# Kernel tuning notes

Measured on AMD Instinct MI355X. Metric: run time of the kernel, lower is better.

## Reference

```python
import jax, jax.numpy as jnp
from jax import lax
import numpy as np

EPS_LN = 1e-5
EPS_BN = 1e-5


def _forward(x, prior, alpha, in_proj_w, conv_w, conv_b, x_proj_weight,
             dt_projs_weight, dt_projs_bias, A_logs, Ds, out_norm_w, out_norm_b,
             out_proj_w, p2w_w1, p2w_b1, p2w_bn_w, p2w_bn_b, p2w_bn_mean,
             p2w_bn_var, p2w_w2, p2w_b2):
    Din = conv_w.shape[0]
    # in_proj (Linear2d == 1x1 conv), split into ssm branch and gate z
    xz = jnp.einsum('bchw,dc->bdhw', x, in_proj_w)          # [B, 2*Din, H, W]
    x_ssm, z = jnp.split(xz, 2, axis=1)
    # depthwise 3x3 conv + SiLU
    x_ssm = lax.conv_general_dilated(
        x_ssm, conv_w, (1, 1), 'SAME',
        dimension_numbers=('NCHW', 'OIHW', 'NCHW'),
        feature_group_count=Din) + conv_b[None, :, None, None]
    x_ssm = jax.nn.silu(x_ssm)

    B, D, H, W = x_ssm.shape
    L = H * W
    K = 4
    R = dt_projs_weight.shape[2]
    N = A_logs.shape[1]

    # cross_scan: 4 directions = row-major, col-major, and their reverses
    row = x_ssm.reshape(B, D, L)
    col = x_ssm.transpose(0, 1, 3, 2).reshape(B, D, L)
    xs = jnp.stack([row, col, row[..., ::-1], col[..., ::-1]], axis=1)  # [B,K,D,L]

    x_dbl = jnp.einsum('bkdl,kcd->bkcl', xs, x_proj_weight)  # [B,K,R+2N,L]
    dts, Bs, Cs = jnp.split(x_dbl, [R, R + N], axis=2)       # [B,K,R,L],[B,K,N,L],[B,K,N,L]
    dts = jnp.einsum('bkrl,kdr->bkdl', dts, dt_projs_weight)  # [B,K,D,L]

    A = -jnp.exp(A_logs.astype(jnp.float32)).reshape(K, D, N)
    dt = jax.nn.softplus(dts + dt_projs_bias[None, :, :, None])  # [B,K,D,L]

    dA = jnp.exp(dt[..., None] * A[None, :, :, None, :])          # [B,K,D,L,N]
    dBx = dt[..., None] * Bs.transpose(0, 1, 3, 2)[:, :, None, :, :] * xs[..., None]
    Cseq = Cs.transpose(0, 1, 3, 2)                               # [B,K,L,N]

    dA_t = jnp.moveaxis(dA, 3, 0)    # [L,B,K,D,N]
    dBx_t = jnp.moveaxis(dBx, 3, 0)  # [L,B,K,D,N]
    C_t = jnp.moveaxis(Cseq, 2, 0)   # [L,B,K,N]

    def step(h, inp):
        a, bx, c = inp
        h = h * a + bx                              # [B,K,D,N]
        y = jnp.einsum('bkdn,bkn->bkd', h, c)
        return h, y

    h0 = jnp.zeros((B, K, D, N), dtype=jnp.float32)
    _, ys = lax.scan(step, h0, (dA_t, dBx_t, C_t))  # [L,B,K,D]
    ys = jnp.moveaxis(ys, 0, 3)                     # [B,K,D,L]
    ys = ys + Ds.reshape(K, D)[None, :, :, None] * xs
    ys = ys.reshape(B, K, D, H, W)

    # prior -> per-direction guidance weights (PriorToWeights, BN in eval mode)
    g = jnp.einsum('bchw,oc->bohw', prior, p2w_w1) + p2w_b1[None, :, None, None]
    g = (g - p2w_bn_mean[None, :, None, None]) * jax.lax.rsqrt(
        p2w_bn_var[None, :, None, None] + EPS_BN)
    g = g * p2w_bn_w[None, :, None, None] + p2w_bn_b[None, :, None, None]
    g = jax.nn.relu(g)
    g = jnp.einsum('bchw,oc->bohw', g, p2w_w2) + p2w_b2[None, :, None, None]
    gw = jax.nn.sigmoid(g)                          # [B,4,H,W]
    s = jax.nn.sigmoid(alpha)                       # [1]
    Wdir = 1.0 + s * (gw - 1.0)                     # torch.lerp(ones, gw, s)
    ys = ys * Wdir[:, :, None, :, :]

    # cross_merge: inverse of cross_scan, sum of 4 directions
    ysl = ys.reshape(B, K, D, L)
    y = ysl[:, 0] + ysl[:, 2, :, ::-1]
    yt = ysl[:, 1] + ysl[:, 3, :, ::-1]
    y = y + yt.reshape(B, D, W, H).transpose(0, 1, 3, 2).reshape(B, D, L)
    y = y.reshape(B, D, H, W)

    # LayerNorm2d: normalize over channel dim
    mu = y.mean(axis=1, keepdims=True)
    var = y.var(axis=1, keepdims=True)
    y = (y - mu) * jax.lax.rsqrt(var + EPS_LN)
    y = y * out_norm_w[None, :, None, None] + out_norm_b[None, :, None, None]

    y = y * jax.nn.silu(z)
    out = jnp.einsum('bdhw,md->bmhw', y, out_proj_w)  # out_proj 1x1, no bias
    return out


def setup_inputs() -> dict:
    key = jax.random.key(0)
    ks = jax.random.split(key, 16)
    B, Dm, H, W = 8, 96, 64, 64
    Din, N, K, R, hid = 192, 1, 4, 6, 32

    def rn(k, shape, scale):
        return jax.random.normal(k, shape, jnp.float32) * scale

    return {
        'x': rn(ks[0], (B, Dm, H, W), 1.0),
        'prior': jax.random.uniform(ks[1], (B, 4, H, W), jnp.float32),
        'alpha': rn(ks[2], (1,), 1.0),
        'in_proj_w': rn(ks[3], (2 * Din, Dm), Dm ** -0.5),
        'conv_w': rn(ks[4], (Din, 1, 3, 3), 1.0 / 3.0),
        'conv_b': rn(ks[5], (Din,), 0.1),
        'x_proj_weight': rn(ks[6], (K, R + 2 * N, Din), Din ** -0.5),
        'dt_projs_weight': rn(ks[7], (K, Din, R), R ** -0.5),
        'dt_projs_bias': rn(ks[8], (K, Din), 0.5) - 4.0,
        'A_logs': jnp.tile(jnp.log(jnp.arange(1, N + 1, dtype=jnp.float32)), (K * Din, 1)),
        'Ds': jnp.ones((K * Din,), jnp.float32),
        'out_norm_w': jnp.ones((Din,), jnp.float32),
        'out_norm_b': jnp.zeros((Din,), jnp.float32),
        'out_proj_w': rn(ks[9], (Dm, Din), Din ** -0.5),
        'p2w_w1': rn(ks[10], (hid, 4), 0.5),
        'p2w_b1': jnp.zeros((hid,), jnp.float32),
        'p2w_bn_w': jnp.ones((hid,), jnp.float32),
        'p2w_bn_b': jnp.zeros((hid,), jnp.float32),
        'p2w_bn_mean': jnp.zeros((hid,), jnp.float32),
        'p2w_bn_var': jnp.ones((hid,), jnp.float32),
        'p2w_w2': rn(ks[11], (4, hid), hid ** -0.5),
        'p2w_b2': jnp.zeros((4,), jnp.float32),
    }


def reference(x, prior, alpha, in_proj_w, conv_w, conv_b, x_proj_weight,
              dt_projs_weight, dt_projs_bias, A_logs, Ds, out_norm_w, out_norm_b,
              out_proj_w, p2w_w1, p2w_b1, p2w_bn_w, p2w_bn_b, p2w_bn_mean,
              p2w_bn_var, p2w_w2, p2w_b2):
    return _forward(x, prior, alpha, in_proj_w, conv_w, conv_b, x_proj_weight,
                    dt_projs_weight, dt_projs_bias, A_logs, Ds, out_norm_w,
                    out_norm_b, out_proj_w, p2w_w1, p2w_b1, p2w_bn_w, p2w_bn_b,
                    p2w_bn_mean, p2w_bn_var, p2w_w2, p2w_b2)
```

## Files before the change

kernel.cpp:

```cpp
#include <hip/hip_runtime.h>

#define BB   8
#define CIN  96
#define DIN  192
#define HH   64
#define WW   64
#define LL   4096
#define KK   4
#define COUT 96
#define SS   128
#define LC   32

#define LOG2E 1.4426950408889634f
#define LN2   0.6931471805599453f

typedef unsigned short bf16t;
typedef float f32x2 __attribute__((ext_vector_type(2)));
typedef float f32x4 __attribute__((ext_vector_type(4)));
typedef short bf16x8s __attribute__((ext_vector_type(8)));

__device__ __forceinline__ f32x2 pkfma(f32x2 a, f32x2 b, f32x2 c) {
#if __has_builtin(__builtin_elementwise_fma)
  return __builtin_elementwise_fma(a, b, c);
#else
  f32x2 r;
  r[0] = fmaf(a[0], b[0], c[0]);
  r[1] = fmaf(a[1], b[1], c[1]);
  return r;
#endif
}

__device__ __forceinline__ float exp2fast(float x) { return __builtin_amdgcn_exp2f(x); }
__device__ __forceinline__ float log2fast(float x) { return __builtin_amdgcn_logf(x); }
__device__ __forceinline__ float sigf(float x) { return 1.0f / (1.0f + __expf(-x)); }
__device__ __forceinline__ int trp(int p) { return ((p & 63) << 6) | (p >> 6); }
__device__ __forceinline__ int pix_of(int k, int l) {
  if (k == 0) return l;
  if (k == 1) return trp(l);
  if (k == 2) return LL - 1 - l;
  return trp(LL - 1 - l);
}
__device__ __forceinline__ float b2f(bf16t v) {
  return __uint_as_float((unsigned)v << 16);
}
__device__ __forceinline__ bf16t f2b(float f) {
  unsigned u = __float_as_uint(f);
  return (bf16t)((u + 0x7FFFu + ((u >> 16) & 1u)) >> 16);
}

__global__ __launch_bounds__(256) void gemm_in_mfma_k(const float* __restrict__ x,
                                                      const bf16t* __restrict__ Wb,
                                                      bf16t* __restrict__ out) {
  __shared__ bf16t ldsB[32 * 104];
  const int tid = threadIdx.x;
  const int b = blockIdx.z;
  const int p0 = blockIdx.x * 32;
  for (int idx = tid; idx < CIN * 32; idx += 256) {
    int c = idx >> 5, px = idx & 31;
    ldsB[px * 104 + c] = f2b(x[((size_t)b * CIN + c) * LL + p0 + px]);
  }
  __syncthreads();
  const int wave = tid >> 6, lane = tid & 63;
  const int lm = lane & 15, kc = lane >> 4;
  bf16x8s bfrag[2][3];
#pragma unroll
  for (int nf = 0; nf < 2; ++nf)
#pragma unroll
    for (int ks = 0; ks < 3; ++ks)
      bfrag[nf][ks] = *(const bf16x8s*)&ldsB[(nf * 16 + lm) * 104 + ks * 32 + kc * 8];
  bf16t* ob = out + (size_t)b * 384 * LL + p0;
#pragma unroll
  for (int mti = 0; mti < 6; ++mti) {
    const int o0 = (wave * 6 + mti) * 16;
    bf16x8s afrag[3];
#pragma unroll
    for (int ks = 0; ks < 3; ++ks)
      afrag[ks] = *(const bf16x8s*)&Wb[(size_t)(o0 + lm) * CIN + ks * 32 + kc * 8];
    f32x4 acc0 = {0.f, 0.f, 0.f, 0.f};
    f32x4 acc1 = {0.f, 0.f, 0.f, 0.f};
#pragma unroll
    for (int ks = 0; ks < 3; ++ks) {
      acc0 = __builtin_amdgcn_mfma_f32_16x16x32_bf16(afrag[ks], bfrag[0][ks], acc0, 0, 0, 0);
      acc1 = __builtin_amdgcn_mfma_f32_16x16x32_bf16(afrag[ks], bfrag[1][ks], acc1, 0, 0, 0);
    }
#pragma unroll
    for (int r = 0; r < 4; ++r) {
      ob[(size_t)(o0 + kc * 4 + r) * LL + lm]      = f2b(acc0[r]);
      ob[(size_t)(o0 + kc * 4 + r) * LL + 16 + lm] = f2b(acc1[r]);
    }
  }
}

__global__ __launch_bounds__(384) void ln_gemm_out_k(const bf16t* __restrict__ ymT,
                                                     const bf16t* __restrict__ ymT2,
                                                     const bf16t* __restrict__ xz,
                                                     const float* __restrict__ gamma,
                                                     const float* __restrict__ beta,
                                                     const bf16t* __restrict__ Wh,
                                                     const bf16t* __restrict__ Wl,
                                                     float* __restrict__ out) {
  __shared__ bf16t ldsB[64 * 200];
  __shared__ float sS[6][64], sQ[6][64];
  const int tid = threadIdx.x;
  const int b = blockIdx.z;
  const int h = blockIdx.x;
  const int p0 = h * 64;
  const bf16t* ymb = ymT + (size_t)b * (384 * (size_t)LL);
  for (int idx = tid; idx < 64 * DIN; idx += 384) {
    int pp = idx / DIN, dd = idx % DIN;
    float v = b2f(ymb[(size_t)(p0 + pp) * DIN + dd]) +
              b2f(ymT2[((size_t)b * LL + pp * 64 + h) * DIN + dd]);
    ldsB[pp * 200 + dd] = f2b(v);
  }
  __syncthreads();
  const int px = tid & 63, g = tid >> 6;
  float sum = 0.0f, ss = 0.0f;
  for (int dd = g * 32; dd < g * 32 + 32; ++dd) {
    float v = b2f(ldsB[px * 200 + dd]);
    sum += v;
    ss = fmaf(v, v, ss);
  }
  sS[g][px] = sum;
  sQ[g][px] = ss;
  __syncthreads();
  sum = 0.0f; ss = 0.0f;
#pragma unroll
  for (int gg = 0; gg < 6; ++gg) { sum += sS[gg][px]; ss += sQ[gg][px]; }
  const float mu = sum * (1.0f / DIN);
  float var = ss * (1.0f / DIN) - mu * mu;
  const float rstd = rsqrtf(fmaxf(var, 0.0f) + 1e-5f);
  const bf16t* zb = xz + ((size_t)b * 384 + DIN) * LL + p0 + px;
  for (int dd = g * 32; dd < g * 32 + 32; ++dd) {
    float v = b2f(ldsB[px * 200 + dd]);
    float z = b2f(zb[(size_t)dd * LL]);
    float tn = fmaf((v - mu) * rstd, gamma[dd], beta[dd]);
    ldsB[px * 200 + dd] = f2b(tn * (z * sigf(z)));
  }
  __syncthreads();
  const int wave = tid / 64, lane = tid & 63;
  const int lm = lane & 15, kc = lane >> 4;
  const int o0 = wave * 16;
  bf16x8s ah[6], al[6];
#pragma unroll
  for (int ks = 0; ks < 6; ++ks) {
    ah[ks] = *(const bf16x8s*)&Wh[(size_t)(o0 + lm) * DIN + ks * 32 + kc * 8];
    al[ks] = *(const bf16x8s*)&Wl[(size_t)(o0 + lm) * DIN + ks * 32 + kc * 8];
  }
  float* ob = out + (size_t)b * COUT * LL + p0;
#pragma unroll
  for (int nf = 0; nf < 4; ++nf) {
    f32x4 acc = {0.f, 0.f, 0.f, 0.f};
#pragma unroll
    for (int ks = 0; ks < 6; ++ks) {
      bf16x8s bfr = *(const bf16x8s*)&ldsB[(nf * 16 + lm) * 200 + ks * 32 + kc * 8];
      acc = __builtin_amdgcn_mfma_f32_16x16x32_bf16(ah[ks], bfr, acc, 0, 0, 0);
      acc = __builtin_amdgcn_mfma_f32_16x16x32_bf16(al[ks], bfr, acc, 0, 0, 0);
    }
#pragma unroll
    for (int r = 0; r < 4; ++r)
      ob[(size_t)(o0 + kc * 4 + r) * LL + nf * 16 + lm] = acc[r];
  }
}

__global__ __launch_bounds__(256) void p2w_k(const float* __restrict__ prior,
                                             const float* __restrict__ alpha,
                                             const float* __restrict__ w1,
                                             const float* __restrict__ b1,
                                             const float* __restrict__ bnw,
                                             const float* __restrict__ bnb,
                                             const float* __restrict__ bnm,
                                             const float* __restrict__ bnv,
                                             const float* __restrict__ w2,
                                             const float* __restrict__ b2,
                                             const float* __restrict__ xpw,
                                             const float* __restrict__ ipw,
                                             const float* __restrict__ opw,
                                             float* __restrict__ xpwT,
                                             bf16t* __restrict__ ipwb,
                                             bf16t* __restrict__ opwbh,
                                             bf16t* __restrict__ opwbl,
                                             float* __restrict__ Wg) {
  if (blockIdx.x == 0) {
    for (int idx = threadIdx.x; idx < KK * DIN * 8; idx += 256) {
      int kk = idx / (DIN * 8);
      int rem = idx % (DIN * 8);
      int dd = rem >> 3, c = rem & 7;
      xpwT[idx] = xpw[(kk * 8 + c) * DIN + dd];
    }
  }
  if (blockIdx.x == 1) {
    for (int idx = threadIdx.x; idx < 384 * CIN; idx += 256)
      ipwb[idx] = f2b(ipw[idx]);
  }
  if (blockIdx.x == 2) {
    for (int idx = threadIdx.x; idx < COUT * DIN; idx += 256) {
      float w = opw[idx];
      bf16t hi = f2b(w);
      opwbh[idx] = hi;
      opwbl[idx] = f2b(w - b2f(hi));
    }
  }
  int idx = blockIdx.x * 256 + threadIdx.x;
  int p = idx & (LL - 1);
  int b = idx >> 12;
  float pr[4];
#pragma unroll
  for (int c = 0; c < 4; ++c) pr[c] = prior[((size_t)b * 4 + c) * LL + p];
  float s = sigf(alpha[0]);
  float g2[4];
#pragma unroll
  for (int j = 0; j < 4; ++j) g2[j] = b2[j];
  for (int o = 0; o < 32; ++o) {
    float g = b1[o];
#pragma unroll
    for (int c = 0; c < 4; ++c) g = fmaf(pr[c], w1[o * 4 + c], g);
    g = (g - bnm[o]) * rsqrtf(bnv[o] + 1e-5f) * bnw[o] + bnb[o];
    g = fmaxf(g, 0.0f);
#pragma unroll
    for (int j = 0; j < 4; ++j) g2[j] = fmaf(g, w2[j * 32 + o], g2[j]);
  }
#pragma unroll
  for (int j = 0; j < 4; ++j)
    Wg[((size_t)b * 4 + j) * LL + p] = 1.0f + s * (sigf(g2[j]) - 1.0f);
}

__global__ __launch_bounds__(1024) void convproj_k(const bf16t* __restrict__ xz,
                                                   const float* __restrict__ cw,
                                                   const float* __restrict__ cb,
                                                   const float* __restrict__ xpwT,
                                                   bf16t* __restrict__ xcT,
                                                   float* __restrict__ projS) {
  __shared__ float sX[96 * 65];
  __shared__ float4 sP[512];
  const int tid = threadIdx.x;
  const int b = blockIdx.y;
  const int h = blockIdx.x;
  const int px = tid & 63;
  const int ku = __builtin_amdgcn_readfirstlane((tid >> 6) & 3);
  const int hf = __builtin_amdgcn_readfirstlane((tid >> 8) & 1);
  const int q  = __builtin_amdgcn_readfirstlane(tid >> 9);
  f32x2 a01 = {0.f, 0.f}, a23 = {0.f, 0.f};

#pragma unroll
  for (int half = 0; half < 2; ++half) {
    for (int idx = tid; idx < 96 * 16; idx += 1024) {
      int ddl = idx >> 4, pq = idx & 15;
      int w0 = pq * 4;
      int dd = half * 96 + ddl;
      const bf16t* base = xz + ((size_t)b * 384 + dd) * LL + h * 64 + w0;
      const float* wp = cw + dd * 9;
      float bv = cb[dd];
      f32x2 s01 = {bv, bv}, s23 = {bv, bv};
#pragma unroll
      for (int dh = -1; dh <= 1; ++dh) {
        int hh = h + dh;
        if (hh < 0 || hh >= HH) continue;
        const bf16t* row = base + dh * 64;
        ushort4 cmu = *(const ushort4*)row;
        float cmx = b2f(cmu.x), cmy = b2f(cmu.y), cmz = b2f(cmu.z), cmw = b2f(cmu.w);
        float lf = (w0 > 0)  ? b2f(row[-1]) : 0.0f;
        float rt = (w0 < 60) ? b2f(row[4])  : 0.0f;
        float c0 = wp[(dh + 1) * 3], c1 = wp[(dh + 1) * 3 + 1], c2 = wp[(dh + 1) * 3 + 2];
        s01 = pkfma((f32x2){lf,  cmx}, (f32x2){c0, c0}, s01);
        s01 = pkfma((f32x2){cmx, cmy}, (f32x2){c1, c1}, s01);
        s01 = pkfma((f32x2){cmy, cmz}, (f32x2){c2, c2}, s01);
        s23 = pkfma((f32x2){cmy, cmz}, (f32x2){c0, c0}, s23);
        s23 = pkfma((f32x2){cmz, cmw}, (f32x2){c1, c1}, s23);
        s23 = pkfma((f32x2){cmw, rt},  (f32x2){c2, c2}, s23);
      }
      float* so = &sX[ddl * 65 + w0];
      float v0 = s01[0], v1 = s01[1], v2 = s23[0], v3 = s23[1];
      so[0] = v0 * sigf(v0);
      so[1] = v1 * sigf(v1);
      so[2] = v2 * sigf(v2);
      so[3] = v3 * sigf(v3);
    }
    __syncthreads();
    for (int idx = tid; idx < 64 * 96; idx += 1024) {
      int pp = idx / 96, ddl = idx % 96;
      xcT[((size_t)b * LL + h * 64 + pp) * DIN + half * 96 + ddl] =
          f2b(sX[ddl * 65 + pp]);
    }
    {
      const int ddl0 = q * 48;
      const float* wp = xpwT + (size_t)ku * (DIN * 8) + (half * 96 + ddl0) * 8 + hf * 4;
#pragma unroll 8
      for (int d48 = 0; d48 < 48; ++d48) {
        float xv = sX[(ddl0 + d48) * 65 + px];
        const float4 w4 = *(const float4*)(wp + d48 * 8);
        const f32x2 xv2 = {xv, xv};
        a01 = pkfma(xv2, (f32x2){w4.x, w4.y}, a01);
        a23 = pkfma(xv2, (f32x2){w4.z, w4.w}, a23);
      }
    }
    __syncthreads();
  }
  const int slot = tid & 511;
  if (q == 1) sP[slot] = make_float4(a01[0], a01[1], a23[0], a23[1]);
  __syncthreads();
  if (q == 0) {
    float4 o = sP[slot];
    float r0 = a01[0] + o.x, r1 = a01[1] + o.y, r2 = a23[0] + o.z, r3 = a23[1] + o.w;
    const int p = h * 64 + px;
    int l;
    if (ku == 0) l = p;
    else if (ku == 1) l = trp(p);
    else if (ku == 2) l = LL - 1 - p;
    else l = LL - 1 - trp(p);
    float* pb = projS + (((size_t)b * KK + ku) * LL + l) * 8 + hf * 4;
    *(float4*)pb = make_float4(r0, r1, r2, r3);
  }
}

__global__ __launch_bounds__(192) void scan_part_k(const bf16t* __restrict__ xcT,
                                                   const float* __restrict__ projS,
                                                   const float* __restrict__ dtw,
                                                   const float* __restrict__ dtb,
                                                   const float* __restrict__ A_logs,
                                                   float* __restrict__ carrP,
                                                   float* __restrict__ carrH) {
  const int s = blockIdx.x, kp = blockIdx.y, b = blockIdx.z;
  const int d = threadIdx.x;
  const int kA = kp, kB = kp + 2;
  const int s2 = SS - 1 - s;
  const int kdA = kA * DIN + d, kdB = kB * DIN + d;
  float wrA[6], wrB[6];
#pragma unroll
  for (int r = 0; r < 6; ++r) { wrA[r] = dtw[kdA * 6 + r]; wrB[r] = dtw[kdB * 6 + r]; }
  const float biasA = dtb[kdA], biasB = dtb[kdB];
  const float AaA = -__expf(A_logs[kdA]), AaB = -__expf(A_logs[kdB]);
  const int l0 = s * LC;
  const int p0 = pix_of(kA, l0);
  const int dp = pix_of(kA, l0 + 1) - p0;
  const bf16t* xp = xcT + ((size_t)b * LL + p0) * DIN + d;
  const long xstep = (long)dp * DIN;
  const float* prA = projS + (((size_t)b * KK + kA) * LL + l0) * 8;
  const float* prB = projS + (((size_t)b * KK + kB) * LL + s2 * LC + (LC - 1)) * 8;
  float PA = 1.0f, HA = 0.0f, PB = 1.0f, HB = 0.0f;
#pragma unroll 2
  for (int j = 0; j < LC; ++j) {
    float4 a0 = *(const float4*)prA;
    float4 a1 = *(const float4*)(prA + 4);
    prA += 8;
    float4 b0 = *(const float4*)prB;
    float4 b1 = *(const float4*)(prB + 4);
    prB -= 8;
    float xv = b2f(*xp);
    xp += xstep;
    {
      float dtr = biasA;
      dtr = fmaf(a0.x, wrA[0], dtr);
      dtr = fmaf(a0.y, wrA[1], dtr);
      dtr = fmaf(a0.z, wrA[2], dtr);
      dtr = fmaf(a0.w, wrA[3], dtr);
      dtr = fmaf(a1.x, wrA[4], dtr);
      dtr = fmaf(a1.y, wrA[5], dtr);
      float e = exp2fast(fminf(dtr, 80.0f) * LOG2E);
      float u = log2fast(1.0f + e);
      float a = exp2fast(u * AaA);
      float dt = u * LN2;
      HA = fmaf(a, HA, dt * a1.z * xv);
      PA *= a;
    }
    {
      float dtr = biasB;
      dtr = fmaf(b0.x, wrB[0], dtr);
      dtr = fmaf(b0.y, wrB[1], dtr);
      dtr = fmaf(b0.z, wrB[2], dtr);
      dtr = fmaf(b0.w, wrB[3], dtr);
      dtr = fmaf(b1.x, wrB[4], dtr);
      dtr = fmaf(b1.y, wrB[5], dtr);
      float e = exp2fast(fminf(dtr, 80.0f) * LOG2E);
      float u = log2fast(1.0f + e);
      float a = exp2fast(u * AaB);
      float dt = u * LN2;
      HB = fmaf(PB, dt * b1.z * xv, HB);
      PB *= a;
    }
  }
  size_t oA = ((size_t)((b * KK + kA) * SS + s)) * DIN + d;
  size_t oB = ((size_t)((b * KK + kB) * SS + s2)) * DIN + d;
  carrP[oA] = PA;
  carrH[oA] = HA;
  carrP[oB] = PB;
  carrH[oB] = HB;
}

__global__ __launch_bounds__(192) void scan_fix_k(const float* __restrict__ carrP,
                                                  const float* __restrict__ carrH,
                                                  float* __restrict__ h0) {
  const int k = blockIdx.x, b = blockIdx.y, d = threadIdx.x;
  size_t base = ((size_t)(b * KK + k)) * SS * DIN + d;
  float h = 0.0f;
#pragma unroll 4
  for (int s = 0; s < SS; ++s) {
    h0[base + (size_t)s * DIN] = h;
    h = fmaf(carrP[base + (size_t)s * DIN], h, carrH[base + (size_t)s * DIN]);
  }
}

__global__ __launch_bounds__(192) void scan_apply_k(const bf16t* __restrict__ xcT,
                                                    const float* __restrict__ projS,
                                                    const float* __restrict__ Wg,
                                                    const float* __restrict__ h0,
                                                    const float* __restrict__ dtw,
                                                    const float* __restrict__ dtb,
                                                    const float* __restrict__ A_logs,
                                                    const float* __restrict__ Ds,
                                                    bf16t* __restrict__ ymT,
                                                    bf16t* __restrict__ ymT2) {
  const int s = blockIdx.x, kp = blockIdx.y, b = blockIdx.z;
  const int d = threadIdx.x;
  __shared__ float sAcc[LC * DIN];
  float xr[LC];
  {
    const int k = kp, kd = k * DIN + d;
    float wr[6];
#pragma unroll
    for (int r = 0; r < 6; ++r) wr[r] = dtw[kd * 6 + r];
    const float bias = dtb[kd];
    const float Aa = -__expf(A_logs[kd]);
    const float Dv = Ds[kd];
    const int l0 = s * LC;
    const int p0 = pix_of(k, l0);
    const int dp = pix_of(k, l0 + 1) - p0;
    const bf16t* xp = xcT + ((size_t)b * LL + p0) * DIN + d;
    const long xstep = (long)dp * DIN;
    const float* pr = projS + (((size_t)b * KK + k) * LL + l0) * 8;
    const float* wg = Wg + ((size_t)b * KK + k) * LL + l0;
    float h = h0[((size_t)((b * KK + k) * SS + s)) * DIN + d];
#pragma unroll
    for (int j = 0; j < LC; ++j) {
      float4 q0 = *(const float4*)pr;
      float4 q1 = *(const float4*)(pr + 4);
      pr += 8;
      float xv = b2f(*xp);
      xp += xstep;
      xr[j] = xv;
      float dtr = bias;
      dtr = fmaf(q0.x, wr[0], dtr);
      dtr = fmaf(q0.y, wr[1], dtr);
      dtr = fmaf(q0.z, wr[2], dtr);
      dtr = fmaf(q0.w, wr[3], dtr);
      dtr = fmaf(q1.x, wr[4], dtr);
      dtr = fmaf(q1.y, wr[5], dtr);
      float e = exp2fast(fminf(dtr, 80.0f) * LOG2E);
      float u = log2fast(1.0f + e);
      float a = exp2fast(u * Aa);
      float dt = u * LN2;
      h = fmaf(a, h, dt * q1.z * xv);
      sAcc[j * DIN + d] = fmaf(h, q1.w, Dv * xv) * wg[j];
    }
  }
  {
    const int k = kp + 2, kd = k * DIN + d;
    const int s2 = SS - 1 - s;
    float wr[6];
#pragma unroll
    for (int r = 0; r < 6; ++r) wr[r] = dtw[kd * 6 + r];
    const float bias = dtb[kd];
    const float Aa = -__expf(A_logs[kd]);
    const float Dv = Ds[kd];
    const int l0 = s2 * LC;
    const float* pr = projS + (((size_t)b * KK + k) * LL + l0) * 8;
    const float* wg = Wg + ((size_t)b * KK + k) * LL + l0;
    float h = h0[((size_t)((b * KK + k) * SS + s2)) * DIN + d];
#pragma unroll
    for (int j = 0; j < LC; ++j) {
      float4 q0 = *(const float4*)pr;
      float4 q1 = *(const float4*)(pr + 4);
      pr += 8;
      float xv = xr[LC - 1 - j];
      float dtr = bias;
      dtr = fmaf(q0.x, wr[0], dtr);
      dtr = fmaf(q0.y, wr[1], dtr);
      dtr = fmaf(q0.z, wr[2], dtr);
      dtr = fmaf(q0.w, wr[3], dtr);
      dtr = fmaf(q1.x, wr[4], dtr);
      dtr = fmaf(q1.y, wr[5], dtr);
      float e = exp2fast(fminf(dtr, 80.0f) * LOG2E);
      float u = log2fast(1.0f + e);
      float a = exp2fast(u * Aa);
      float dt = u * LN2;
      h = fmaf(a, h, dt * q1.z * xv);
      float y = fmaf(h, q1.w, Dv * xv) * wg[j];
      sAcc[(LC - 1 - j) * DIN + d] += y;
    }
  }
  bf16t* dst;
  if (kp == 0)
    dst = ymT + (size_t)b * (384 * (size_t)LL) + (size_t)(s * LC) * DIN + d;
  else
    dst = ymT2 + ((size_t)b * LL + s * LC) * DIN + d;
#pragma unroll 4
  for (int j = 0; j < LC; ++j) dst[(size_t)j * DIN] = f2b(sAcc[j * DIN + d]);
}

extern "C" void kernel_launch(void* const* d_in, const int* in_sizes, int n_in,
                              void* d_out, int out_size, void* d_ws, size_t ws_size,
                              hipStream_t stream) {
  const float* x      = (const float*)d_in[0];
  const float* prior  = (const float*)d_in[1];
  const float* alpha  = (const float*)d_in[2];
  const float* ipw    = (const float*)d_in[3];
  const float* cw     = (const float*)d_in[4];
  const float* cb     = (const float*)d_in[5];
  const float* xpw    = (const float*)d_in[6];
  const float* dtw    = (const float*)d_in[7];
  const float* dtb    = (const float*)d_in[8];
  const float* A_logs = (const float*)d_in[9];
  const float* Ds     = (const float*)d_in[10];
  const float* onw    = (const float*)d_in[11];
  const float* onb    = (const float*)d_in[12];
  const float* opw    = (const float*)d_in[13];
  const float* w1     = (const float*)d_in[14];
  const float* b1     = (const float*)d_in[15];
  const float* bnw    = (const float*)d_in[16];
  const float* bnb    = (const float*)d_in[17];
  const float* bnm    = (const float*)d_in[18];
  const float* bnv    = (const float*)d_in[19];
  const float* w2     = (const float*)d_in[20];
  const float* b2     = (const float*)d_in[21];
  float* out = (float*)d_out;

  char* ws = (char*)d_ws;
  bf16t* xz    = (bf16t*)(ws);
  bf16t* xcT   = (bf16t*)(ws + 25165824);
  bf16t* ymT2  = (bf16t*)(ws + 37748736);
  float* projS = (float*)(ws + 50331648);
  float* Wgb   = (float*)(ws + 54525952);
  float* carrP = (float*)(ws + 55050240);
  float* carrH = (float*)(ws + 58195968);
  float* h0b   = (float*)(ws + 61341696);
  float* xpwT  = (float*)(ws + 64487424);
  bf16t* ipwb  = (bf16t*)(ws + 64512000);
  bf16t* opwbh = (bf16t*)(ws + 64585728);
  bf16t* opwbl = (bf16t*)(ws + 64622592);
  bf16t* ymT   = xz;

  p2w_k<<<(BB * LL) / 256, 256, 0, stream>>>(prior, alpha, w1, b1, bnw, bnb, bnm,
                                             bnv, w2, b2, xpw, ipw, opw, xpwT,
                                             ipwb, opwbh, opwbl, Wgb);
  gemm_in_mfma_k<<<dim3(LL / 32, 1, BB), 256, 0, stream>>>(x, ipwb, xz);
  convproj_k<<<dim3(HH, BB), 1024, 0, stream>>>(xz, cw, cb, xpwT, xcT, projS);
  scan_part_k<<<dim3(SS, 2, BB), 192, 0, stream>>>(xcT, projS, dtw, dtb, A_logs,
                                                   carrP, carrH);
  scan_fix_k<<<dim3(KK, BB), 192, 0, stream>>>(carrP, carrH, h0b);
  scan_apply_k<<<dim3(SS, 2, BB), 192, 0, stream>>>(xcT, projS, Wgb, h0b, dtw, dtb,
                                                    A_logs, Ds, ymT, ymT2);
  ln_gemm_out_k<<<dim3(LL / 64, 1, BB), 384, 0, stream>>>(ymT, ymT2, xz, onw, onb,
                                                          opwbh, opwbl, out);
}
```

Baseline: 154.3 us.

## Compute x_proj with bf16 MFMA using hi/lo weight split in convproj

Replaces the scalar packed-FMA x_proj projection in convproj_k with bf16 MFMA 16x16x32 instructions. The x_proj weights are split into bf16 high and low parts to keep accuracy close to fp32 on the weight side. The activations are staged once as bf16 in shared memory, laid out pixel-major, and that tile feeds both the vectorised xcT store and the MFMA B operand. The block shrinks from 1024 to 512 threads and the two-half loop plus cross-half reduction go away. In exchange the activations are rounded to bf16 before the projection, and projS is now written with scalar stores.

```diff
diff --git a/kernel.cpp b/kernel.cpp
--- a/kernel.cpp
+++ b/kernel.cpp
@@ -175,17 +175,18 @@
                                              const float* __restrict__ xpw,
                                              const float* __restrict__ ipw,
                                              const float* __restrict__ opw,
-                                             float* __restrict__ xpwT,
+                                             bf16t* __restrict__ xpwbh,
+                                             bf16t* __restrict__ xpwbl,
                                              bf16t* __restrict__ ipwb,
                                              bf16t* __restrict__ opwbh,
                                              bf16t* __restrict__ opwbl,
                                              float* __restrict__ Wg) {
   if (blockIdx.x == 0) {
-    for (int idx = threadIdx.x; idx < KK * DIN * 8; idx += 256) {
-      int kk = idx / (DIN * 8);
-      int rem = idx % (DIN * 8);
-      int dd = rem >> 3, c = rem & 7;
-      xpwT[idx] = xpw[(kk * 8 + c) * DIN + dd];
+    for (int idx = threadIdx.x; idx < 32 * DIN; idx += 256) {
+      float w = xpw[idx];
+      bf16t hi = f2b(w);
+      xpwbh[idx] = hi;
+      xpwbl[idx] = f2b(w - b2f(hi));
     }
   }
   if (blockIdx.x == 1) {
@@ -224,91 +225,81 @@
     Wg[((size_t)b * 4 + j) * LL + p] = 1.0f + s * (sigf(g2[j]) - 1.0f);
 }
 
-__global__ __launch_bounds__(1024) void convproj_k(const bf16t* __restrict__ xz,
-                                                   const float* __restrict__ cw,
-                                                   const float* __restrict__ cb,
-                                                   const float* __restrict__ xpwT,
-                                                   bf16t* __restrict__ xcT,
-                                                   float* __restrict__ projS) {
-  __shared__ float sX[96 * 65];
-  __shared__ float4 sP[512];
+__global__ __launch_bounds__(512) void convproj_k(const bf16t* __restrict__ xz,
+                                                  const float* __restrict__ cw,
+                                                  const float* __restrict__ cb,
+                                                  const bf16t* __restrict__ Wh,
+                                                  const bf16t* __restrict__ Wl,
+                                                  bf16t* __restrict__ xcT,
+                                                  float* __restrict__ projS) {
+  __shared__ bf16t sXb[64 * 200];
   const int tid = threadIdx.x;
   const int b = blockIdx.y;
   const int h = blockIdx.x;
-  const int px = tid & 63;
-  const int ku = __builtin_amdgcn_readfirstlane((tid >> 6) & 3);
-  const int hf = __builtin_amdgcn_readfirstlane((tid >> 8) & 1);
-  const int q  = __builtin_amdgcn_readfirstlane(tid >> 9);
-  f32x2 a01 = {0.f, 0.f}, a23 = {0.f, 0.f};
-
-#pragma unroll
-  for (int half = 0; half < 2; ++half) {
-    for (int idx = tid; idx < 96 * 16; idx += 1024) {
-      int ddl = idx >> 4, pq = idx & 15;
-      int w0 = pq * 4;
-      int dd = half * 96 + ddl;
-      const bf16t* base = xz + ((size_t)b * 384 + dd) * LL + h * 64 + w0;
-      const float* wp = cw + dd * 9;
-      float bv = cb[dd];
-      f32x2 s01 = {bv, bv}, s23 = {bv, bv};
-#pragma unroll
-      for (int dh = -1; dh <= 1; ++dh) {
-        int hh = h + dh;
-        if (hh < 0 || hh >= HH) continue;
-        const bf16t* row = base + dh * 64;
-        ushort4 cmu = *(const ushort4*)row;
-        float cmx = b2f(cmu.x), cmy = b2f(cmu.y), cmz = b2f(cmu.z), cmw = b2f(cmu.w);
-        float lf = (w0 > 0)  ? b2f(row[-1]) : 0.0f;
-        float rt = (w0 < 60) ? b2f(row[4])  : 0.0f;
-        float c0 = wp[(dh + 1) * 3], c1 = wp[(dh + 1) * 3 + 1], c2 = wp[(dh + 1) * 3 + 2];
-        s01 = pkfma((f32x2){lf,  cmx}, (f32x2){c0, c0}, s01);
-        s01 = pkfma((f32x2){cmx, cmy}, (f32x2){c1, c1}, s01);
-        s01 = pkfma((f32x2){cmy, cmz}, (f32x2){c2, c2}, s01);
-        s23 = pkfma((f32x2){cmy, cmz}, (f32x2){c0, c0}, s23);
-        s23 = pkfma((f32x2){cmz, cmw}, (f32x2){c1, c1}, s23);
-        s23 = pkfma((f32x2){cmw, rt},  (f32x2){c2, c2}, s23);
-      }
-      float* so = &sX[ddl * 65 + w0];
-      float v0 = s01[0], v1 = s01[1], v2 = s23[0], v3 = s23[1];
-      so[0] = v0 * sigf(v0);
-      so[1] = v1 * sigf(v1);
-      so[2] = v2 * sigf(v2);
-      so[3] = v3 * sigf(v3);
-    }
-    __syncthreads();
-    for (int idx = tid; idx < 64 * 96; idx += 1024) {
-      int pp = idx / 96, ddl = idx % 96;
-      xcT[((size_t)b * LL + h * 64 + pp) * DIN + half * 96 + ddl] =
-          f2b(sX[ddl * 65 + pp]);
-    }
-    {
-      const int ddl0 = q * 48;
-      const float* wp = xpwT + (size_t)ku * (DIN * 8) + (half * 96 + ddl0) * 8 + hf * 4;
-#pragma unroll 8
-      for (int d48 = 0; d48 < 48; ++d48) {
-        float xv = sX[(ddl0 + d48) * 65 + px];
-        const float4 w4 = *(const float4*)(wp + d48 * 8);
-        const f32x2 xv2 = {xv, xv};
-        a01 = pkfma(xv2, (f32x2){w4.x, w4.y}, a01);
-        a23 = pkfma(xv2, (f32x2){w4.z, w4.w}, a23);
-      }
-    }
-    __syncthreads();
-  }
-  const int slot = tid & 511;
-  if (q == 1) sP[slot] = make_float4(a01[0], a01[1], a23[0], a23[1]);
+  for (int idx = tid; idx < DIN * 16; idx += 512) {
+    int dd = idx >> 4, pq = idx & 15;
+    int w0 = pq * 4;
+    const bf16t* base = xz + ((size_t)b * 384 + dd) * LL + h * 64 + w0;
+    const float* wp = cw + dd * 9;
+    float bv = cb[dd];
+    f32x2 s01 = {bv, bv}, s23 = {bv, bv};
+#pragma unroll
+    for (int dh = -1; dh <= 1; ++dh) {
+      int hh = h + dh;
+      if (hh < 0 || hh >= HH) continue;
+      const bf16t* row = base + dh * 64;
+      ushort4 cmu = *(const ushort4*)row;
+      float cmx = b2f(cmu.x), cmy = b2f(cmu.y), cmz = b2f(cmu.z), cmw = b2f(cmu.w);
+      float lf = (w0 > 0)  ? b2f(row[-1]) : 0.0f;
+      float rt = (w0 < 60) ? b2f(row[4])  : 0.0f;
+      float c0 = wp[(dh + 1) * 3], c1 = wp[(dh + 1) * 3 + 1], c2 = wp[(dh + 1) * 3 + 2];
+      s01 = pkfma((f32x2){lf,  cmx}, (f32x2){c0, c0}, s01);
+      s01 = pkfma((f32x2){cmx, cmy}, (f32x2){c1, c1}, s01);
+      s01 = pkfma((f32x2){cmy, cmz}, (f32x2){c2, c2}, s01);
+      s23 = pkfma((f32x2){cmy, cmz}, (f32x2){c0, c0}, s23);
+      s23 = pkfma((f32x2){cmz, cmw}, (f32x2){c1, c1}, s23);
+      s23 = pkfma((f32x2){cmw, rt},  (f32x2){c2, c2}, s23);
+    }
+    float v0 = s01[0], v1 = s01[1], v2 = s23[0], v3 = s23[1];
+    sXb[(w0 + 0) * 200 + dd] = f2b(v0 * sigf(v0));
+    sXb[(w0 + 1) * 200 + dd] = f2b(v1 * sigf(v1));
+    sXb[(w0 + 2) * 200 + dd] = f2b(v2 * sigf(v2));
+    sXb[(w0 + 3) * 200 + dd] = f2b(v3 * sigf(v3));
+  }
   __syncthreads();
-  if (q == 0) {
-    float4 o = sP[slot];
-    float r0 = a01[0] + o.x, r1 = a01[1] + o.y, r2 = a23[0] + o.z, r3 = a23[1] + o.w;
-    const int p = h * 64 + px;
+  for (int idx = tid; idx < 64 * (DIN / 4); idx += 512) {
+    int pp = idx / 48, dq = idx % 48;
+    *(ushort4*)&xcT[((size_t)b * LL + h * 64 + pp) * DIN + dq * 4] =
+        *(const ushort4*)&sXb[pp * 200 + dq * 4];
+  }
+  const int wave = tid >> 6, lane = tid & 63;
+  const int lm = lane & 15, kc = lane >> 4;
+  const int mti = wave >> 2, nf = wave & 3;
+  bf16x8s ah[6], al[6], bfr[6];
+#pragma unroll
+  for (int ks = 0; ks < 6; ++ks) {
+    ah[ks] = *(const bf16x8s*)&Wh[(size_t)(mti * 16 + lm) * DIN + ks * 32 + kc * 8];
+    al[ks] = *(const bf16x8s*)&Wl[(size_t)(mti * 16 + lm) * DIN + ks * 32 + kc * 8];
+    bfr[ks] = *(const bf16x8s*)&sXb[(nf * 16 + lm) * 200 + ks * 32 + kc * 8];
+  }
+  f32x4 acc = {0.f, 0.f, 0.f, 0.f};
+#pragma unroll
+  for (int ks = 0; ks < 6; ++ks) {
+    acc = __builtin_amdgcn_mfma_f32_16x16x32_bf16(ah[ks], bfr[ks], acc, 0, 0, 0);
+    acc = __builtin_amdgcn_mfma_f32_16x16x32_bf16(al[ks], bfr[ks], acc, 0, 0, 0);
+  }
+  const int px = nf * 16 + lm;
+  const int p = h * 64 + px;
+#pragma unroll
+  for (int r = 0; r < 4; ++r) {
+    int o = mti * 16 + kc * 4 + r;
+    int k = o >> 3, c = o & 7;
     int l;
-    if (ku == 0) l = p;
-    else if (ku == 1) l = trp(p);
-    else if (ku == 2) l = LL - 1 - p;
+    if (k == 0) l = p;
+    else if (k == 1) l = trp(p);
+    else if (k == 2) l = LL - 1 - p;
     else l = LL - 1 - trp(p);
-    float* pb = projS + (((size_t)b * KK + ku) * LL + l) * 8 + hf * 4;
-    *(float4*)pb = make_float4(r0, r1, r2, r3);
+    projS[(((size_t)b * KK + k) * LL + l) * 8 + c] = acc[r];
   }
 }
 
@@ -532,17 +523,18 @@
   float* carrP = (float*)(ws + 55050240);
   float* carrH = (float*)(ws + 58195968);
   float* h0b   = (float*)(ws + 61341696);
-  float* xpwT  = (float*)(ws + 64487424);
+  bf16t* xpwbh = (bf16t*)(ws + 64487424);
+  bf16t* xpwbl = (bf16t*)(ws + 64499712);
   bf16t* ipwb  = (bf16t*)(ws + 64512000);
   bf16t* opwbh = (bf16t*)(ws + 64585728);
   bf16t* opwbl = (bf16t*)(ws + 64622592);
   bf16t* ymT   = xz;
 
   p2w_k<<<(BB * LL) / 256, 256, 0, stream>>>(prior, alpha, w1, b1, bnw, bnb, bnm,
-                                             bnv, w2, b2, xpw, ipw, opw, xpwT,
-                                             ipwb, opwbh, opwbl, Wgb);
+                                             bnv, w2, b2, xpw, ipw, opw, xpwbh,
+                                             xpwbl, ipwb, opwbh, opwbl, Wgb);
   gemm_in_mfma_k<<<dim3(LL / 32, 1, BB), 256, 0, stream>>>(x, ipwb, xz);
-  convproj_k<<<dim3(HH, BB), 1024, 0, stream>>>(xz, cw, cb, xpwT, xcT, projS);
+  convproj_k<<<dim3(HH, BB), 512, 0, stream>>>(xz, cw, cb, xpwbh, xpwbl, xcT, projS);
   scan_part_k<<<dim3(SS, 2, BB), 192, 0, stream>>>(xcT, projS, dtw, dtb, A_logs,
                                                    carrP, carrH);
   scan_fix_k<<<dim3(KK, BB), 192, 0, stream>>>(carrP, carrH, h0b);
```

Measured after the change: 159.0 us. 1.03x slower.
